# Kernel tuning notes

Hardware: AMD Instinct MI355X
Metric: run time of the kernel (lower is better)

The kernel has to match this reference:

```python
import jax, jax.numpy as jnp
import numpy as np

NUM_GROUPS = 32
RANK = 64            # per-head rank (uniform)
IN_FEATURES = 4096
OUT_FEATURES = 4096
GROUP_DIM = OUT_FEATURES // NUM_GROUPS  # 128
SUM_RANKS = NUM_GROUPS * RANK           # 2048


def setup_inputs() -> dict:
    key = jax.random.key(0)
    k1, k2, k3 = jax.random.split(key, 3)
    hidden_states = jax.random.normal(k1, (4, 4096, IN_FEATURES), dtype=jnp.float32)
    # VT: nn.Linear(in_features, sum(ranks), bias=False) -> weight [sum_ranks, in]
    VT_weight = jax.random.normal(k2, (SUM_RANKS, IN_FEATURES), dtype=jnp.float32) * (1.0 / np.sqrt(IN_FEATURES))
    # U_list: per-group nn.Linear(r, group_dim), init.normal_ -> stacked [G, group_dim, r]
    U_weight = jax.random.normal(k3, (NUM_GROUPS, GROUP_DIM, RANK), dtype=jnp.float32)
    return {"hidden_states": hidden_states, "VT_weight": VT_weight, "U_weight": U_weight}


def reference(hidden_states, VT_weight, U_weight):
    # shared down-projection: [B,S,in] @ [in,sum_ranks] -> [B,S,sum_ranks]
    z = jnp.einsum('bsi,ri->bsr', hidden_states, VT_weight)
    B, S, _ = z.shape
    # grouped up-projection (block-diagonal GEMM): slice per group -> [B,S,G,r]
    zg = z.reshape(B, S, NUM_GROUPS, RANK)
    out = jnp.einsum('bsgr,gdr->bsgd', zg, U_weight)  # [B,S,G,group_dim]
    return out.reshape(B, S, NUM_GROUPS * GROUP_DIM)  # concat along last dim
```

## Files before the change

kernel.cpp:

```cpp
#include <hip/hip_runtime.h>
#include <hip/hip_bf16.h>
#include <stdint.h>

typedef __attribute__((ext_vector_type(8)))  short bf16x8;
typedef __attribute__((ext_vector_type(4)))  float f32x4;
typedef __attribute__((ext_vector_type(4)))  float float4v;
typedef __attribute__((ext_vector_type(8)))  unsigned short u16x8;

#define MFMA16(a,b,c) __builtin_amdgcn_mfma_f32_16x16x32_bf16((a),(b),(c),0,0,0)

__device__ __forceinline__ unsigned short f2bf(float f) {
    unsigned int u = __builtin_bit_cast(unsigned int, f);
    u = (u + 0x7fffu + ((u >> 16) & 1u)) >> 16;
    return (unsigned short)u;
}

__device__ __forceinline__ void gload_lds16(const void* g, void* l) {
    __builtin_amdgcn_global_load_lds(
        (const __attribute__((address_space(1))) void*)g,
        (__attribute__((address_space(3))) void*)l, 16, 0, 0);
}

template<int N> __device__ __forceinline__ void waitvm() {}
template<> __device__ __forceinline__ void waitvm<6>() { asm volatile("s_waitcnt vmcnt(6)" ::: "memory"); }
template<> __device__ __forceinline__ void waitvm<4>() { asm volatile("s_waitcnt vmcnt(4)" ::: "memory"); }
template<> __device__ __forceinline__ void waitvm<0>() { asm volatile("s_waitcnt vmcnt(0)" ::: "memory"); }

__global__ void cvt_f32_bf16(const float* __restrict__ in, unsigned short* __restrict__ out, long n) {
    long i = ((long)blockIdx.x * blockDim.x + threadIdx.x) * 8;
    long stride = (long)gridDim.x * blockDim.x * 8;
    for (; i < n; i += stride) {
        float4v v0 = *(const float4v*)(in + i);
        float4v v1 = *(const float4v*)(in + i + 4);
        u16x8 o;
        o[0] = f2bf(v0[0]); o[1] = f2bf(v0[1]); o[2] = f2bf(v0[2]); o[3] = f2bf(v0[3]);
        o[4] = f2bf(v1[0]); o[5] = f2bf(v1[1]); o[6] = f2bf(v1[2]); o[7] = f2bf(v1[3]);
        *(u16x8*)(out + i) = o;
    }
}


#define STAGE_A(nA_, k0n, h, l) \
    gload_lds16(pA + ((l)*128 + (h)*64) * 4096L + (k0n), (nA_) + dA0 + ((l)*128 + (h)*64) * 64)
#define STAGE_B(nB_, k0n, h, l) \
    gload_lds16(pB + ((l)*128 + (h)*32) * 4096L + (k0n), (nB_) + dB0 + ((l)*128 + (h)*32) * 64)

#define LDA(dst_, sA_, QM) do { _Pragma("unroll") for (int mi = 0; mi < 4; ++mi) { \
    dst_[mi][0] = *(const bf16x8*)((sA_) + ((wr*128 + (QM)*64 + mi*16 + lan15) << 6) + g0); \
    dst_[mi][1] = *(const bf16x8*)((sA_) + ((wr*128 + (QM)*64 + mi*16 + lan15) << 6) + (g0 ^ 32)); } } while (0)
#define LDB(dst_, sB_, QN) do { _Pragma("unroll") for (int ni = 0; ni < 2; ++ni) { \
    dst_[ni][0] = *(const bf16x8*)((sB_) + ((wc*64 + (QN)*32 + ni*16 + lan15) << 6) + g0); \
    dst_[ni][1] = *(const bf16x8*)((sB_) + ((wc*64 + (QN)*32 + ni*16 + lan15) << 6) + (g0 ^ 32)); } } while (0)

#define DOMFMA(QM, QN, aset_, bset_) do { __builtin_amdgcn_s_setprio(1); \
    _Pragma("unroll") for (int mi = 0; mi < 4; ++mi) \
      _Pragma("unroll") for (int ni = 0; ni < 2; ++ni) { \
        acc[(QM)*4+mi][(QN)*2+ni] = MFMA16(aset_[mi][0], bset_[ni][0], acc[(QM)*4+mi][(QN)*2+ni]); \
        acc[(QM)*4+mi][(QN)*2+ni] = MFMA16(aset_[mi][1], bset_[ni][1], acc[(QM)*4+mi][(QN)*2+ni]); } \
    __builtin_amdgcn_s_setprio(0); } while (0)

#define BAR1() do { __builtin_amdgcn_s_barrier(); \
    asm volatile("s_waitcnt lgkmcnt(0)" ::: "memory"); \
    __builtin_amdgcn_sched_barrier(0); } while (0)
#define BAR2() do { __builtin_amdgcn_s_barrier(); \
    __builtin_amdgcn_sched_barrier(0); } while (0)

#define ITER8(K1, K2, K3, S2, S3, T8, V3, V7) do { \
   STAGE_A(bA1, K1, 1, 0); STAGE_A(bA1, K1, 1, 1); \
         BAR1(); DOMFMA(0, 0, aE, b0); LDB(b1, bB0, 1); BAR2(); \
   if (S2) { STAGE_A(bA0, K2, 0, 0); STAGE_A(bA0, K2, 0, 1); } \
         BAR1(); DOMFMA(0, 1, aE, b1); LDA(aO, bA0, 1); BAR2(); \
   if (S2) { STAGE_B(bB0, K2, 0, 0); STAGE_B(bB0, K2, 0, 1); } \
         BAR1(); DOMFMA(1, 1, aO, b1); waitvm<V3>(); BAR2(); \
   if (S2) { STAGE_B(bB0, K2, 1, 0); STAGE_B(bB0, K2, 1, 1); } \
         BAR1(); DOMFMA(1, 0, aO, b0); LDA(aE, bA1, 0); LDB(b0, bB1, 0); BAR2(); \
   if (S2) { STAGE_A(bA0, K2, 1, 0); STAGE_A(bA0, K2, 1, 1); } \
         BAR1(); DOMFMA(0, 0, aE, b0); LDB(b1, bB1, 1); BAR2(); \
   if (S3) { STAGE_A(bA1, K3, 0, 0); STAGE_A(bA1, K3, 0, 1); } \
         BAR1(); DOMFMA(0, 1, aE, b1); LDA(aO, bA1, 1); BAR2(); \
   if (S3) { STAGE_B(bB1, K3, 0, 0); STAGE_B(bB1, K3, 0, 1); } \
         BAR1(); DOMFMA(1, 1, aO, b1); waitvm<V7>(); BAR2(); \
   if (S3) { STAGE_B(bB1, K3, 1, 0); STAGE_B(bB1, K3, 1, 1); } \
         BAR1(); DOMFMA(1, 0, aO, b0); \
         if (T8) { LDA(aE, bA0, 0); LDB(b0, bB0, 0); } BAR2(); \
} while (0)

__global__ __launch_bounds__(512, 2) void gemm1_8ph(const unsigned short* __restrict__ A,
                                                    const unsigned short* __restrict__ B,
                                                    unsigned short* __restrict__ Z) {
    __shared__ __align__(16) unsigned short lds[65536];

    const int tid   = threadIdx.x;
    const int lane  = tid & 63;
    const int wid   = tid >> 6;
    const int wr    = wid >> 2;
    const int wc    = wid & 3;
    const int lan15 = lane & 15;
    const int g0    = (((lane >> 4) ^ (lane & 7)) << 3);

    const int  bid = blockIdx.x;
    const long m0  = (long)(bid >> 3) * 256;
    const long n0  = (long)(bid & 7) * 256;

    const int q8    = tid >> 3;
    const int granA = (((tid & 7) ^ (q8 & 7)) << 3);
    const unsigned short* pA = A + (m0 + q8) * 4096L + granA;
    const int rB0   = (q8 & 31) + ((q8 >> 5) << 6);
    const unsigned short* pB = B + (n0 + rB0) * 4096L + granA;
    const int dA0   = (wid * 8) * 64;
    const int dB0   = ((wid & 3) * 8 + ((wid >> 2) << 6)) * 64;

    f32x4 acc[8][4] = {};
    bf16x8 aE[4][2], aO[4][2], b0[2][2], b1[2][2];

    unsigned short* bA0 = lds;
    unsigned short* bB0 = lds + 16384;
    unsigned short* bA1 = lds + 32768;
    unsigned short* bB1 = lds + 49152;

    STAGE_A(bA0, 0, 0, 0);  STAGE_A(bA0, 0, 0, 1);
    STAGE_B(bB0, 0, 0, 0);  STAGE_B(bB0, 0, 0, 1);
    STAGE_B(bB0, 0, 1, 0);  STAGE_B(bB0, 0, 1, 1);
    STAGE_A(bA0, 0, 1, 0);  STAGE_A(bA0, 0, 1, 1);
    STAGE_A(bA1, 64, 0, 0); STAGE_A(bA1, 64, 0, 1);
    STAGE_B(bB1, 64, 0, 0); STAGE_B(bB1, 64, 0, 1);
    STAGE_B(bB1, 64, 1, 0); STAGE_B(bB1, 64, 1, 1);
    waitvm<6>();
    BAR2();
    LDA(aE, bA0, 0); LDB(b0, bB0, 0);

    for (int i = 0; i < 31; ++i) {
        ITER8((2 * i + 1) * 64, (2 * i + 2) * 64, (2 * i + 3) * 64,
              true, true, true, 4, 4);
    }
    ITER8(63 * 64, 0, 0, false, false, false, 0, -1);

    const int rq = (lane >> 4) << 2;
    #pragma unroll
    for (int mi = 0; mi < 8; ++mi) {
        #pragma unroll
        for (int ni = 0; ni < 4; ++ni) {
            const long mb  = m0 + wr * 128 + mi * 16 + rq;
            const long nb2 = n0 + wc * 64 + ni * 16 + lan15;
            #pragma unroll
            for (int j = 0; j < 4; ++j)
                Z[(mb + j) * 2048L + nb2] = f2bf(acc[mi][ni][j]);
        }
    }
}

#define U_PAD 80

__global__ __launch_bounds__(256) void gemm2(const unsigned short* __restrict__ Z,
                                             const float* __restrict__ U,
                                             float* __restrict__ out) {
    __shared__ __align__(16) unsigned short lU[128 * U_PAD];

    const int tid  = threadIdx.x;
    const int lane = tid & 63;
    const int wid  = tid >> 6;
    const int g    = blockIdx.x & 31;
    const long m0  = (long)(blockIdx.x >> 5) * 64;

    const float* ug = U + (long)g * (128 * 64);
    for (int i = tid; i < (128 * 64) / 4; i += 256) {
        const int r = i >> 4;
        const int c = (i << 2) & 63;
        float4v v = *(const float4v*)(ug + i * 4);
        unsigned short* d = &lU[r * U_PAD + c];
        d[0] = f2bf(v[0]); d[1] = f2bf(v[1]); d[2] = f2bf(v[2]); d[3] = f2bf(v[3]);
    }
    __syncthreads();

    const long mrow = m0 + wid * 16 + (lane & 15);
    const unsigned short* zrow = Z + mrow * 2048L + g * 64 + ((lane >> 4) << 3);
    const bf16x8 a0 = *(const bf16x8*)(zrow);
    const bf16x8 a1 = *(const bf16x8*)(zrow + 32);

    f32x4 acc[8] = {};
    const int blds = (lane & 15);
    const int kofs = (lane >> 4) << 3;
    #pragma unroll
    for (int ni = 0; ni < 8; ++ni) {
        const bf16x8 c0 = *(const bf16x8*)&lU[(ni * 16 + blds) * U_PAD + kofs];
        const bf16x8 c1 = *(const bf16x8*)&lU[(ni * 16 + blds) * U_PAD + 32 + kofs];
        acc[ni] = MFMA16(a0, c0, acc[ni]);
        acc[ni] = MFMA16(a1, c1, acc[ni]);
    }

    const long mb = m0 + wid * 16 + ((lane >> 4) << 2);
    const long cb = (long)g * 128 + (lane & 15);
    #pragma unroll
    for (int ni = 0; ni < 8; ++ni)
        #pragma unroll
        for (int j = 0; j < 4; ++j)
            out[(mb + j) * 4096L + cb + ni * 16] = acc[ni][j];
}

extern "C" void kernel_launch(void* const* d_in, const int* in_sizes, int n_in,
                              void* d_out, int out_size, void* d_ws, size_t ws_size,
                              hipStream_t stream) {
    const float* hs = (const float*)d_in[0];
    const float* vt = (const float*)d_in[1];
    const float* uw = (const float*)d_in[2];
    float* out = (float*)d_out;

    unsigned short* hs_bf = (unsigned short*)d_ws;
    unsigned short* vt_bf = hs_bf + 67108864L;
    unsigned short* z_bf  = vt_bf + 8388608L;

    cvt_f32_bf16<<<2048, 256, 0, stream>>>(hs, hs_bf, 67108864L);
    cvt_f32_bf16<<<512, 256, 0, stream>>>(vt, vt_bf, 8388608L);

    gemm1_8ph<<<512, 512, 0, stream>>>(hs_bf, vt_bf, z_bf);

    gemm2<<<8192, 256, 0, stream>>>(z_bf, uw, out);
}
```

Before: 362.3 us.

## Halve per-phase barriers and regroup LDS staging in the 8-phase GEMM pipeline

Each pipeline phase of the down-projection GEMM previously had two workgroup barriers. This change keeps only the leading barrier, which also waits on lgkmcnt, and replaces the trailing one with a scheduling barrier. The A and B global-to-LDS staging that used to sit in separate phases is merged into one phase, placed after the LDS reads of the other half. The aim is to cut barrier stall time between MFMA groups. The cost is a weaker guarantee against LDS write-after-read races between waves.

```diff
diff --git a/kernel.cpp b/kernel.cpp
--- a/kernel.cpp
+++ b/kernel.cpp
@@ -59,30 +59,29 @@
         acc[(QM)*4+mi][(QN)*2+ni] = MFMA16(aset_[mi][1], bset_[ni][1], acc[(QM)*4+mi][(QN)*2+ni]); } \
     __builtin_amdgcn_s_setprio(0); } while (0)
 
-#define BAR1() do { __builtin_amdgcn_s_barrier(); \
+#define BARX() do { __builtin_amdgcn_s_barrier(); \
     asm volatile("s_waitcnt lgkmcnt(0)" ::: "memory"); \
     __builtin_amdgcn_sched_barrier(0); } while (0)
-#define BAR2() do { __builtin_amdgcn_s_barrier(); \
-    __builtin_amdgcn_sched_barrier(0); } while (0)
+#define SB() __builtin_amdgcn_sched_barrier(0)
 
 #define ITER8(K1, K2, K3, S2, S3, T8, V3, V7) do { \
    STAGE_A(bA1, K1, 1, 0); STAGE_A(bA1, K1, 1, 1); \
-         BAR1(); DOMFMA(0, 0, aE, b0); LDB(b1, bB0, 1); BAR2(); \
-   if (S2) { STAGE_A(bA0, K2, 0, 0); STAGE_A(bA0, K2, 0, 1); } \
-         BAR1(); DOMFMA(0, 1, aE, b1); LDA(aO, bA0, 1); BAR2(); \
-   if (S2) { STAGE_B(bB0, K2, 0, 0); STAGE_B(bB0, K2, 0, 1); } \
-         BAR1(); DOMFMA(1, 1, aO, b1); waitvm<V3>(); BAR2(); \
+         BARX(); DOMFMA(0, 0, aE, b0); LDB(b1, bB0, 1); SB(); \
+   BARX(); DOMFMA(0, 1, aE, b1); LDA(aO, bA0, 1); SB(); \
+   if (S2) { STAGE_A(bA0, K2, 0, 0); STAGE_A(bA0, K2, 0, 1); \
+                   STAGE_B(bB0, K2, 0, 0); STAGE_B(bB0, K2, 0, 1); } \
+         BARX(); DOMFMA(1, 1, aO, b1); waitvm<V3>(); SB(); \
    if (S2) { STAGE_B(bB0, K2, 1, 0); STAGE_B(bB0, K2, 1, 1); } \
-         BAR1(); DOMFMA(1, 0, aO, b0); LDA(aE, bA1, 0); LDB(b0, bB1, 0); BAR2(); \
+         BARX(); DOMFMA(1, 0, aO, b0); LDA(aE, bA1, 0); LDB(b0, bB1, 0); SB(); \
    if (S2) { STAGE_A(bA0, K2, 1, 0); STAGE_A(bA0, K2, 1, 1); } \
-         BAR1(); DOMFMA(0, 0, aE, b0); LDB(b1, bB1, 1); BAR2(); \
-   if (S3) { STAGE_A(bA1, K3, 0, 0); STAGE_A(bA1, K3, 0, 1); } \
-         BAR1(); DOMFMA(0, 1, aE, b1); LDA(aO, bA1, 1); BAR2(); \
-   if (S3) { STAGE_B(bB1, K3, 0, 0); STAGE_B(bB1, K3, 0, 1); } \
-         BAR1(); DOMFMA(1, 1, aO, b1); waitvm<V7>(); BAR2(); \
+         BARX(); DOMFMA(0, 0, aE, b0); LDB(b1, bB1, 1); SB(); \
+   BARX(); DOMFMA(0, 1, aE, b1); LDA(aO, bA1, 1); SB(); \
+   if (S3) { STAGE_A(bA1, K3, 0, 0); STAGE_A(bA1, K3, 0, 1); \
+                   STAGE_B(bB1, K3, 0, 0); STAGE_B(bB1, K3, 0, 1); } \
+         BARX(); DOMFMA(1, 1, aO, b1); waitvm<V7>(); SB(); \
    if (S3) { STAGE_B(bB1, K3, 1, 0); STAGE_B(bB1, K3, 1, 1); } \
-         BAR1(); DOMFMA(1, 0, aO, b0); \
-         if (T8) { LDA(aE, bA0, 0); LDB(b0, bB0, 0); } BAR2(); \
+         BARX(); DOMFMA(1, 0, aO, b0); \
+         if (T8) { LDA(aE, bA0, 0); LDB(b0, bB0, 0); } SB(); \
 } while (0)
 
 __global__ __launch_bounds__(512, 2) void gemm1_8ph(const unsigned short* __restrict__ A,
@@ -126,8 +125,10 @@
     STAGE_B(bB1, 64, 0, 0); STAGE_B(bB1, 64, 0, 1);
     STAGE_B(bB1, 64, 1, 0); STAGE_B(bB1, 64, 1, 1);
     waitvm<6>();
-    BAR2();
+    __builtin_amdgcn_s_barrier();
+    __builtin_amdgcn_sched_barrier(0);
     LDA(aE, bA0, 0); LDB(b0, bB0, 0);
+    SB();
 
     for (int i = 0; i < 31; ++i) {
         ITER8((2 * i + 1) * 64, (2 * i + 2) * 64, (2 * i + 3) * 64,
```

Result: no change. 357.2 us (-1.4%).
